# Performance work log

Hardware: AMD Instinct MI355X
Metric: run time of the kernel (lower is better)

Reference implementation:

```python
import jax, jax.numpy as jnp
import numpy as np

TAU = 0.1
LAM = 1.0
LOG_NOISE = 1e-12
COS_EPS = 1e-8      # torch CosineSimilarity eps
NORM_EPS = 1e-12    # torch F.normalize eps


def setup_inputs() -> dict:
    key = jax.random.key(0)
    k1, k2, k3, k4 = jax.random.split(key, 4)
    B, D, S = 8192, 128, 64
    z1s = jax.random.normal(k1, (B, D), dtype=jnp.float32)
    z2s = jax.random.normal(k2, (B, D), dtype=jnp.float32)
    z1_c_outs = jax.random.uniform(k3, (B, S), dtype=jnp.float32)
    z1_subject_labels = jax.random.normal(k4, (B, S), dtype=jnp.float32)
    return {"z1s": z1s, "z2s": z2s, "z1_c_outs": z1_c_outs,
            "z1_subject_labels": z1_subject_labels}


def _l2_normalize(x, eps):
    # normalize rows; clamp norm from below like torch
    n = jnp.linalg.norm(x, axis=1, keepdims=True)
    return x / jnp.maximum(n, eps)


def reference(z1s, z2s, z1_c_outs, z1_subject_labels):
    B = z1s.shape[0]
    z1 = z1s.reshape(B, -1)
    z2 = z2s.reshape(B, -1)
    n1 = _l2_normalize(z1, COS_EPS)
    n2 = _l2_normalize(z2, COS_EPS)

    # all-pairs cosine similarities, scaled by temperature
    S12 = jnp.matmul(n1, n2.T) / TAU   # [B, B] sim(z1_i, z2_k)/tau
    S11 = jnp.matmul(n1, n1.T) / TAU   # [B, B] sim(z1_i, z1_k)/tau

    e12 = jnp.exp(S12)
    e11 = jnp.exp(S11)
    numerator = jnp.diagonal(e12)                       # exp(sim(z1_i, z2_i)/tau)
    # denom_i = sum_k e12[i,k] + sum_{k != i} e11[i,k]
    denom = e12.sum(axis=1) + e11.sum(axis=1) - jnp.diagonal(e11)
    contrastive = -jnp.log(LOG_NOISE + numerator / denom)
    loss = contrastive.sum() / (B * (2.0 * B - 1.0))

    # adversarial term: -lam * log(1 - normalized_pred[i, argmax(label_i)])
    c = _l2_normalize(z1_c_outs, NORM_EPS)
    j = jnp.argmax(z1_subject_labels, axis=1)           # [B] int
    picked = c[jnp.arange(B), j]
    loss = loss + LAM * (-jnp.log(LOG_NOISE + 1.0 - picked)).sum()
    return loss
```

## Files before the change

kernel.cpp:

```cpp
#include <hip/hip_runtime.h>
#include <hip/hip_bf16.h>
#include <math.h>


#define NROWS 8192
#define DFEAT 128

typedef __bf16 bf16_t;
typedef __bf16 bf16x8 __attribute__((ext_vector_type(8)));
typedef __bf16 bf16x2 __attribute__((ext_vector_type(2)));
typedef float  f32x4  __attribute__((ext_vector_type(4)));

__device__ __forceinline__ float fexp2(float x) {
#if __has_builtin(__builtin_amdgcn_exp2f)
  return __builtin_amdgcn_exp2f(x);
#else
  return exp2f(x);
#endif
}

__device__ __forceinline__ void stage16(const void* gsrc, void* ldst) {
  __builtin_amdgcn_global_load_lds(
      (const __attribute__((address_space(1))) unsigned int*)gsrc,
      (__attribute__((address_space(3))) unsigned int*)ldst, 16, 0, 0);
}

__global__ __launch_bounds__(256)
void sa_prep_kernel(const float* __restrict__ z1,
                    const float* __restrict__ z2,
                    bf16_t* __restrict__ Abuf,
                    bf16_t* __restrict__ Kc,
                    float* __restrict__ numv,
                    float* __restrict__ d11v) {
  int wave = threadIdx.x >> 6;
  int lane = threadIdx.x & 63;
  int row  = blockIdx.x * 4 + wave;

  const float2* z1p = (const float2*)(z1 + row * DFEAT);
  const float2* z2p = (const float2*)(z2 + row * DFEAT);
  float2 a = z1p[lane];
  float2 b = z2p[lane];

  float s1  = a.x * a.x + a.y * a.y;
  float s2  = b.x * b.x + b.y * b.y;
  float s12 = a.x * b.x + a.y * b.y;
#pragma unroll
  for (int m = 32; m; m >>= 1) {
    s1  += __shfl_xor(s1, m, 64);
    s2  += __shfl_xor(s2, m, 64);
    s12 += __shfl_xor(s12, m, 64);
  }
  float r1 = 1.0f / fmaxf(sqrtf(s1), 1e-8f);
  float r2 = 1.0f / fmaxf(sqrtf(s2), 1e-8f);

  const float SCL = 14.426950408889634f;

  bf16x2 av;  av[0] = (bf16_t)(a.x * r1 * SCL); av[1] = (bf16_t)(a.y * r1 * SCL);
  bf16x2 k2v; k2v[0] = (bf16_t)(b.x * r2);      k2v[1] = (bf16_t)(b.y * r2);
  bf16x2 k1v; k1v[0] = (bf16_t)(a.x * r1);      k1v[1] = (bf16_t)(a.y * r1);

  int tile = row >> 4;
  int l15c = row & 15;
  int kf   = lane >> 4;
  int qk   = (lane >> 2) & 3;
  int jj   = (lane & 3) * 2;
  size_t fo = ((size_t)qk * 16 + l15c) * 8 + jj;

  *(bf16x2*)(Abuf + (size_t)(tile * 4 + kf) * 512 + fo)         = av;
  *(bf16x2*)(Kc   + (size_t)(tile * 4 + kf) * 512 + fo)         = k2v;
  *(bf16x2*)(Kc   + (size_t)((512 + tile) * 4 + kf) * 512 + fo) = k1v;

  if (lane == 0) {
    numv[row] = expf(10.0f * s12 * r1 * r2);
    d11v[row] = expf(10.0f * s1 * r1 * r1);
  }
}

__global__ __launch_bounds__(256, 4)
void sa_main_kernel(const bf16_t* __restrict__ Abuf,
                    const bf16_t* __restrict__ Kc,
                    float* __restrict__ T2) {
  __shared__ __align__(16) bf16_t bsm[2][2048];

  int wave = threadIdx.x >> 6;
  int lane = threadIdx.x & 63;
  int quad = lane >> 4;

  int id  = blockIdx.x;
  int swz = (id & 7) * 128 + (id >> 3);
  int bx  = swz & 31;
  int by  = swz >> 5;
  int rowBase = bx * 256 + wave * 64;
  int colBase = by * 512;

  const bf16x8* ap = (const bf16x8*)Abuf + (size_t)(rowBase >> 4) * 256 + lane;
  bf16x8 afrag[4][4];
#pragma unroll
  for (int s = 0; s < 4; ++s)
#pragma unroll
    for (int kfi = 0; kfi < 4; ++kfi)
      afrag[s][kfi] = ap[(s * 4 + kfi) * 64];

  f32x4 sums[4];
#pragma unroll
  for (int s = 0; s < 4; ++s) sums[s] = (f32x4){0.f, 0.f, 0.f, 0.f};

  const char* bsrc = (const char*)Kc + (size_t)(colBase >> 4) * 4096 +
                     (size_t)wave * 1024 + (size_t)lane * 16;
  char* l0 = (char*)&bsm[0][0] + wave * 1024;
  char* l1 = (char*)&bsm[1][0] + wave * 1024;

  stage16(bsrc, l0);
  asm volatile("s_waitcnt vmcnt(0)" ::: "memory");
  __builtin_amdgcn_s_barrier();
  __builtin_amdgcn_sched_barrier(0);

#pragma unroll 1
  for (int it = 0; it < 32; ++it) {
    if (it + 1 < 32)
      stage16(bsrc + (size_t)(it + 1) * 4096, (it & 1) ? l0 : l1);

    const bf16x8* bs = (const bf16x8*)&bsm[it & 1][0];
    bf16x8 bfr[4];
#pragma unroll
    for (int kfi = 0; kfi < 4; ++kfi) bfr[kfi] = bs[kfi * 64 + lane];

#pragma unroll
    for (int s = 0; s < 4; ++s) {
      f32x4 c = {0.f, 0.f, 0.f, 0.f};
#pragma unroll
      for (int kfi = 0; kfi < 4; ++kfi)
        c = __builtin_amdgcn_mfma_f32_16x16x32_bf16(afrag[s][kfi], bfr[kfi], c,
                                                    0, 0, 0);
#pragma unroll
      for (int r = 0; r < 4; ++r) sums[s][r] += fexp2(c[r]);
    }

    asm volatile("s_waitcnt vmcnt(0)" ::: "memory");
    __builtin_amdgcn_s_barrier();
    __builtin_amdgcn_sched_barrier(0);
  }

  int l15 = lane & 15;
#pragma unroll
  for (int s = 0; s < 4; ++s) {
#pragma unroll
    for (int r = 0; r < 4; ++r) {
      float v = sums[s][r];
      v += __shfl_xor(v, 1, 64);
      v += __shfl_xor(v, 2, 64);
      v += __shfl_xor(v, 4, 64);
      v += __shfl_xor(v, 8, 64);
      if (l15 == 0)
        T2[(size_t)(rowBase + s * 16 + quad * 4 + r) * 32 + by] = v;
    }
  }
}

__global__ __launch_bounds__(256)
void sa_final_adv_kernel(const float* __restrict__ T2,
                         const float* __restrict__ numv,
                         const float* __restrict__ d11v,
                         const float* __restrict__ c,
                         const float* __restrict__ lab,
                         float* __restrict__ partial) {
  int wave = threadIdx.x >> 6;
  int lane = threadIdx.x & 63;
  int row  = blockIdx.x * 4 + wave;

  float cv = c[row * 64 + lane];
  float lv = lab[row * 64 + lane];
  float tv = (lane < 32) ? T2[(size_t)row * 32 + lane] : 0.0f;

  float ss = cv * cv;
  float bestv = lv;
  int   besti = lane;
#pragma unroll
  for (int m = 32; m; m >>= 1) {
    ss += __shfl_xor(ss, m, 64);
    tv += __shfl_xor(tv, m, 64);
    float ov = __shfl_xor(bestv, m, 64);
    int   oi = __shfl_xor(besti, m, 64);
    if (ov > bestv || (ov == bestv && oi < besti)) { bestv = ov; besti = oi; }
  }
  float picked = __shfl(cv, besti, 64) / fmaxf(sqrtf(ss), 1e-12f);

  float term = 0.0f;
  if (lane == 0) {
    float denom = tv - d11v[row];
    term = -logf(1e-12f + numv[row] / denom) * (1.0f / 134209536.0f)
           - logf(1e-12f + 1.0f - picked);
  }

  __shared__ float wacc[4];
  if (lane == 0) wacc[wave] = term;
  __syncthreads();
  if (threadIdx.x == 0)
    partial[blockIdx.x] = wacc[0] + wacc[1] + wacc[2] + wacc[3];
}

__global__ __launch_bounds__(256)
void sa_reduce_kernel(const float* __restrict__ partial,
                      float* __restrict__ out) {
  float v = 0.0f;
#pragma unroll
  for (int i = 0; i < 8; ++i) v += partial[threadIdx.x + 256 * i];
#pragma unroll
  for (int m = 32; m; m >>= 1) v += __shfl_xor(v, m, 64);
  __shared__ float wacc[4];
  if ((threadIdx.x & 63) == 0) wacc[threadIdx.x >> 6] = v;
  __syncthreads();
  if (threadIdx.x == 0) out[0] = wacc[0] + wacc[1] + wacc[2] + wacc[3];
}

extern "C" void kernel_launch(void* const* d_in, const int* in_sizes, int n_in,
                              void* d_out, int out_size, void* d_ws,
                              size_t ws_size, hipStream_t stream) {
  const float* z1  = (const float*)d_in[0];
  const float* z2  = (const float*)d_in[1];
  const float* co  = (const float*)d_in[2];
  const float* lab = (const float*)d_in[3];
  float* out = (float*)d_out;

  char* ws = (char*)d_ws;
  bf16_t* Abuf  = (bf16_t*)ws;
  bf16_t* Kc    = (bf16_t*)(ws + 2u * 1024 * 1024);
  float*  T2    = (float*)(ws + 6u * 1024 * 1024);
  float*  numv  = (float*)(ws + 7u * 1024 * 1024);
  float*  d11v  = numv + NROWS;
  float*  part  = d11v + NROWS;

  sa_prep_kernel<<<NROWS / 4, 256, 0, stream>>>(z1, z2, Abuf, Kc, numv, d11v);
  sa_main_kernel<<<1024, 256, 0, stream>>>(Abuf, Kc, T2);
  sa_final_adv_kernel<<<NROWS / 4, 256, 0, stream>>>(T2, numv, d11v, co, lab,
                                                     part);
  sa_reduce_kernel<<<1, 256, 0, stream>>>(part, out);
}
```

Baseline: 111.5 us.

## Deepen main-kernel B staging to a 4-buffer pipeline and coalesce prep stores via LDS

The main kernel now stages two column tiles per phase into a 4-deep LDS ring with three phases in flight. It waits with partial vmcnt instead of draining all loads every iteration, which halves the barriers and hides global-load latency behind the MFMA and exp work. MFMA sections are wrapped in setprio. The prep kernel processes 16 rows per block, transposes through LDS, and writes 16-byte coalesced fragment stores instead of scattered 4-byte ones. LDS use per main block grows from 8 KB to 32 KB, which may reduce occupancy.

```diff
diff --git a/kernel.cpp b/kernel.cpp
--- a/kernel.cpp
+++ b/kernel.cpp
@@ -25,21 +25,26 @@
       (__attribute__((address_space(3))) unsigned int*)ldst, 16, 0, 0);
 }
 
-__global__ __launch_bounds__(256)
+#define WAITVM(n) asm volatile("s_waitcnt vmcnt(" #n ")" ::: "memory")
+
+__global__ __launch_bounds__(1024)
 void sa_prep_kernel(const float* __restrict__ z1,
                     const float* __restrict__ z2,
                     bf16_t* __restrict__ Abuf,
                     bf16_t* __restrict__ Kc,
                     float* __restrict__ numv,
                     float* __restrict__ d11v) {
+  __shared__ __align__(16) bf16_t LA[16][136];
+  __shared__ __align__(16) bf16_t LK2[16][136];
+  __shared__ __align__(16) bf16_t LK1[16][136];
+
   int wave = threadIdx.x >> 6;
   int lane = threadIdx.x & 63;
-  int row  = blockIdx.x * 4 + wave;
-
-  const float2* z1p = (const float2*)(z1 + row * DFEAT);
-  const float2* z2p = (const float2*)(z2 + row * DFEAT);
-  float2 a = z1p[lane];
-  float2 b = z2p[lane];
+  int tile = blockIdx.x;
+  int row  = tile * 16 + wave;
+
+  float2 a = ((const float2*)(z1 + (size_t)row * DFEAT))[lane];
+  float2 b = ((const float2*)(z2 + (size_t)row * DFEAT))[lane];
 
   float s1  = a.x * a.x + a.y * a.y;
   float s2  = b.x * b.x + b.y * b.y;
@@ -59,20 +64,30 @@
   bf16x2 k2v; k2v[0] = (bf16_t)(b.x * r2);      k2v[1] = (bf16_t)(b.y * r2);
   bf16x2 k1v; k1v[0] = (bf16_t)(a.x * r1);      k1v[1] = (bf16_t)(a.y * r1);
 
-  int tile = row >> 4;
-  int l15c = row & 15;
-  int kf   = lane >> 4;
-  int qk   = (lane >> 2) & 3;
-  int jj   = (lane & 3) * 2;
-  size_t fo = ((size_t)qk * 16 + l15c) * 8 + jj;
-
-  *(bf16x2*)(Abuf + (size_t)(tile * 4 + kf) * 512 + fo)         = av;
-  *(bf16x2*)(Kc   + (size_t)(tile * 4 + kf) * 512 + fo)         = k2v;
-  *(bf16x2*)(Kc   + (size_t)((512 + tile) * 4 + kf) * 512 + fo) = k1v;
+  *(bf16x2*)&LA[wave][2 * lane]  = av;
+  *(bf16x2*)&LK2[wave][2 * lane] = k2v;
+  *(bf16x2*)&LK1[wave][2 * lane] = k1v;
 
   if (lane == 0) {
     numv[row] = expf(10.0f * s12 * r1 * r2);
     d11v[row] = expf(10.0f * s1 * r1 * r1);
+  }
+  __syncthreads();
+
+  int t = threadIdx.x;
+  if (t < 768) {
+    int sel = t >> 8;
+    int u   = t & 255;
+    int kf  = u >> 6;
+    int qk  = (u >> 4) & 3;
+    int r16 = u & 15;
+    const bf16_t* Ls = (sel == 0) ? &LA[0][0]
+                     : (sel == 1) ? &LK2[0][0] : &LK1[0][0];
+    bf16x8 v = *(const bf16x8*)(Ls + r16 * 136 + kf * 32 + qk * 8);
+    bf16_t* dst = (sel == 0) ? (Abuf + (size_t)tile * 2048)
+                : (sel == 1) ? (Kc + (size_t)tile * 2048)
+                             : (Kc + (size_t)(512 + tile) * 2048);
+    *(bf16x8*)(dst + u * 8) = v;
   }
 }
 
@@ -80,7 +95,7 @@
 void sa_main_kernel(const bf16_t* __restrict__ Abuf,
                     const bf16_t* __restrict__ Kc,
                     float* __restrict__ T2) {
-  __shared__ __align__(16) bf16_t bsm[2][2048];
+  __shared__ __align__(16) bf16_t bsm[4][4096];
 
   int wave = threadIdx.x >> 6;
   int lane = threadIdx.x & 63;
@@ -106,40 +121,63 @@
   for (int s = 0; s < 4; ++s) sums[s] = (f32x4){0.f, 0.f, 0.f, 0.f};
 
   const char* bsrc = (const char*)Kc + (size_t)(colBase >> 4) * 4096 +
-                     (size_t)wave * 1024 + (size_t)lane * 16;
-  char* l0 = (char*)&bsm[0][0] + wave * 1024;
-  char* l1 = (char*)&bsm[1][0] + wave * 1024;
-
-  stage16(bsrc, l0);
-  asm volatile("s_waitcnt vmcnt(0)" ::: "memory");
+                     (size_t)wave * 2048 + (size_t)lane * 16;
+  char* lbase = (char*)&bsm[0][0] + (size_t)wave * 2048;
+
+  auto stagePhase = [&](int p) {
+    const char* src = bsrc + (size_t)p * 8192;
+    char* dst = lbase + (size_t)(p & 3) * 8192;
+    stage16(src, dst);
+    stage16(src + 1024, dst + 1024);
+  };
+
+  auto computePhase = [&](int pbuf) {
+    const bf16_t* base = &bsm[0][0] + pbuf * 4096;
+#pragma unroll
+    for (int tt = 0; tt < 2; ++tt) {
+      const bf16x8* bs = (const bf16x8*)(base + tt * 2048);
+      bf16x8 bfr[4];
+#pragma unroll
+      for (int kfi = 0; kfi < 4; ++kfi) bfr[kfi] = bs[kfi * 64 + lane];
+      __builtin_amdgcn_s_setprio(1);
+#pragma unroll
+      for (int s = 0; s < 4; ++s) {
+        f32x4 c = {0.f, 0.f, 0.f, 0.f};
+#pragma unroll
+        for (int kfi = 0; kfi < 4; ++kfi)
+          c = __builtin_amdgcn_mfma_f32_16x16x32_bf16(afrag[s][kfi], bfr[kfi],
+                                                      c, 0, 0, 0);
+#pragma unroll
+        for (int r = 0; r < 4; ++r) sums[s][r] += fexp2(c[r]);
+      }
+      __builtin_amdgcn_s_setprio(0);
+    }
+  };
+
+  stagePhase(0);
+  stagePhase(1);
+  stagePhase(2);
+
+#pragma unroll 1
+  for (int p = 0; p < 13; ++p) {
+    WAITVM(4);
+    __builtin_amdgcn_s_barrier();
+    __builtin_amdgcn_sched_barrier(0);
+    stagePhase(p + 3);
+    computePhase(p & 3);
+  }
+  WAITVM(4);
   __builtin_amdgcn_s_barrier();
   __builtin_amdgcn_sched_barrier(0);
-
-#pragma unroll 1
-  for (int it = 0; it < 32; ++it) {
-    if (it + 1 < 32)
-      stage16(bsrc + (size_t)(it + 1) * 4096, (it & 1) ? l0 : l1);
-
-    const bf16x8* bs = (const bf16x8*)&bsm[it & 1][0];
-    bf16x8 bfr[4];
-#pragma unroll
-    for (int kfi = 0; kfi < 4; ++kfi) bfr[kfi] = bs[kfi * 64 + lane];
-
-#pragma unroll
-    for (int s = 0; s < 4; ++s) {
-      f32x4 c = {0.f, 0.f, 0.f, 0.f};
-#pragma unroll
-      for (int kfi = 0; kfi < 4; ++kfi)
-        c = __builtin_amdgcn_mfma_f32_16x16x32_bf16(afrag[s][kfi], bfr[kfi], c,
-                                                    0, 0, 0);
-#pragma unroll
-      for (int r = 0; r < 4; ++r) sums[s][r] += fexp2(c[r]);
-    }
-
-    asm volatile("s_waitcnt vmcnt(0)" ::: "memory");
-    __builtin_amdgcn_s_barrier();
-    __builtin_amdgcn_sched_barrier(0);
-  }
+  computePhase(1);
+  WAITVM(2);
+  __builtin_amdgcn_s_barrier();
+  __builtin_amdgcn_sched_barrier(0);
+  computePhase(2);
+  WAITVM(0);
+  __builtin_amdgcn_s_barrier();
+  __builtin_amdgcn_sched_barrier(0);
+  computePhase(3);
 
   int l15 = lane & 15;
 #pragma unroll
@@ -230,7 +268,8 @@
   float*  d11v  = numv + NROWS;
   float*  part  = d11v + NROWS;
 
-  sa_prep_kernel<<<NROWS / 4, 256, 0, stream>>>(z1, z2, Abuf, Kc, numv, d11v);
+  sa_prep_kernel<<<NROWS / 16, 1024, 0, stream>>>(z1, z2, Abuf, Kc, numv,
+                                                  d11v);
   sa_main_kernel<<<1024, 256, 0, stream>>>(Abuf, Kc, T2);
   sa_final_adv_kernel<<<NROWS / 4, 256, 0, stream>>>(T2, numv, d11v, co, lab,
                                                      part);
```

New measurement: 129.2 us. +15.9%, slower.
